# Optimization experiments

Measured on AMD Instinct MI355X. Metric: run time of the kernel, lower is better.

Reference implementation:

```python
import jax, jax.numpy as jnp
import numpy as np

D_MODEL = 1024
N_HEADS = 16
HEAD_DIM = D_MODEL // N_HEADS
SCALE = float(np.sqrt(HEAD_DIM))
NEG_INF = -1e30


def setup_inputs() -> dict:
    key = jax.random.key(0)
    k1, k2, k3 = jax.random.split(key, 3)
    B, S = 4, 2048
    x = jax.random.normal(k1, (B, S, D_MODEL), dtype=jnp.float32)
    attention_mask = jnp.ones((B, S), dtype=jnp.int32)
    # torch Linear(d, 3d, bias=False): y = x @ W^T; store pre-transposed (d, 3d)
    w_qkv = jax.random.normal(k2, (D_MODEL, 3 * D_MODEL), dtype=jnp.float32) * (1.0 / np.sqrt(D_MODEL))
    w_out = jax.random.normal(k3, (D_MODEL, D_MODEL), dtype=jnp.float32) * (1.0 / np.sqrt(D_MODEL))
    return {"x": x, "attention_mask": attention_mask, "w_qkv": w_qkv, "w_out": w_out}


def reference(x, attention_mask, w_qkv, w_out):
    B, S, _ = x.shape
    qkv = jnp.einsum('bsd,de->bse', x, w_qkv)                     # (B,S,3D)
    qkv = qkv.reshape(B, S, 3, N_HEADS, HEAD_DIM)
    q = qkv[:, :, 0].transpose(0, 2, 1, 3)                        # (B,H,S,hd)
    k = qkv[:, :, 1].transpose(0, 2, 1, 3)
    v = qkv[:, :, 2].transpose(0, 2, 1, 3)

    scores = jnp.einsum('bhqd,bhkd->bhqk', q, k) / SCALE          # (B,H,S,S)
    causal_mask = jnp.triu(jnp.ones((S, S), dtype=bool), k=1)     # True above diag
    scores = jnp.where(causal_mask[None, None], NEG_INF, scores)
    pad_mask = (attention_mask == 0)[:, None, None, :]            # (B,1,1,S)
    scores = jnp.where(pad_mask, NEG_INF, scores)

    attn = jax.nn.softmax(scores, axis=-1)                        # dropout=0 (eval)
    out = jnp.einsum('bhqk,bhkd->bhqd', attn, v)                  # (B,H,S,hd)
    out = out.transpose(0, 2, 1, 3).reshape(B, S, D_MODEL)
    return jnp.einsum('bsd,de->bse', out, w_out)
```

## Files before the change

kernel.cpp:

```cpp
#include <hip/hip_runtime.h>


typedef __attribute__((ext_vector_type(8))) short bf16x8;
typedef __attribute__((ext_vector_type(8))) unsigned short u16x8;
typedef __attribute__((ext_vector_type(4))) unsigned short u16x4;
typedef __attribute__((ext_vector_type(4))) float f32x4;

#define MFMA16 __builtin_amdgcn_mfma_f32_16x16x32_bf16

#define GLDS(gp, lp) __builtin_amdgcn_global_load_lds( \
    (const __attribute__((address_space(1))) unsigned int*)(gp), \
    (__attribute__((address_space(3))) unsigned int*)(lp), 16, 0, 0)

__device__ __forceinline__ unsigned short f2bf(float f) {
    union { float f; unsigned int u; } v; v.f = f;
    unsigned int r = v.u + 0x7fffu + ((v.u >> 16) & 1u);
    return (unsigned short)(r >> 16);
}

__global__ void k_prep(const float* __restrict__ x, unsigned short* __restrict__ xb,
                       const int* __restrict__ mask, unsigned short* __restrict__ mb,
                       const float* __restrict__ wqkv, unsigned short* __restrict__ w1t,
                       const float* __restrict__ wout, unsigned short* __restrict__ w2t) {
    __shared__ float tile[32][33];
    const int bx = blockIdx.x;
    if (bx < 4096) {
        size_t i = ((size_t)bx * 256 + threadIdx.x) * 8;
        float4 f0 = *(const float4*)(x + i);
        float4 f1 = *(const float4*)(x + i + 4);
        u16x8 v;
        v[0] = f2bf(f0.x); v[1] = f2bf(f0.y); v[2] = f2bf(f0.z); v[3] = f2bf(f0.w);
        v[4] = f2bf(f1.x); v[5] = f2bf(f1.y); v[6] = f2bf(f1.z); v[7] = f2bf(f1.w);
        *(u16x8*)(xb + i) = v;
        if (bx < 32) {
            int j = bx * 256 + threadIdx.x;
            mb[j] = mask[j] ? (unsigned short)0x3F80 : (unsigned short)0;
        }
    } else {
        const int b2 = bx - 4096;
        const int cb = b2 & 127, rb = b2 >> 7;
        const float* in = (cb < 96) ? wqkv : wout;
        unsigned short* out = (cb < 96) ? w1t : w2t;
        const int C = (cb < 96) ? 3072 : 1024;
        const int c0 = ((cb < 96) ? cb : cb - 96) * 32;
        const int r0 = rb * 32;
        int tx = threadIdx.x & 31, ty = threadIdx.x >> 5;
        for (int i = ty; i < 32; i += 8)
            tile[i][tx] = in[(size_t)(r0 + i) * C + (c0 + tx)];
        __syncthreads();
        for (int i = ty; i < 32; i += 8)
            out[(size_t)(c0 + i) * 1024 + (r0 + tx)] = f2bf(tile[tx][i]);
    }
}

template <int MODE>
__global__ __launch_bounds__(256) void k_gemm_bt(
    const unsigned short* __restrict__ Ab,
    const unsigned short* __restrict__ Bt,
    float* __restrict__ Cf,
    unsigned short* __restrict__ qb,
    unsigned short* __restrict__ kb,
    unsigned short* __restrict__ vt,
    const int* __restrict__ mask,
    int N, int K)
{
    __shared__ __align__(16) unsigned short la[128 * 64];
    __shared__ __align__(16) unsigned short lb[128 * 64];
    const int t = threadIdx.x;
    const int m0 = blockIdx.y * 128, n0 = blockIdx.x * 128;
    const int w = t >> 6, lane = t & 63;
    const int wm = (w & 1) * 64, wn = (w >> 1) * 64;
    const int lr = lane & 15, lq = lane >> 4;
    const int lr7 = lr & 7;
    const int rowb = lane >> 3;
    const int g8 = (((lane & 7) - rowb) & 7) * 8;

    f32x4 acc[4][4];
    for (int i = 0; i < 4; ++i)
        for (int j = 0; j < 4; ++j)
            acc[i][j] = (f32x4){0.f, 0.f, 0.f, 0.f};

    for (int k0 = 0; k0 < K; k0 += 64) {
        #pragma unroll
        for (int r = 0; r < 4; ++r) {
            const int rg = w * 8 + r * 32;
            GLDS(&Ab[(size_t)(m0 + rg + rowb) * K + k0 + g8], &la[rg * 64]);
            GLDS(&Bt[(size_t)(n0 + rg + rowb) * K + k0 + g8], &lb[rg * 64]);
        }
        __syncthreads();
        #pragma unroll
        for (int ks = 0; ks < 2; ++ks) {
            const int pa = ((ks * 4 + lq + lr7) & 7) * 8;
            bf16x8 af[4], bg[4];
            #pragma unroll
            for (int i = 0; i < 4; ++i) {
                af[i] = *(const bf16x8*)&la[(wm + i * 16 + lr) * 64 + pa];
                bg[i] = *(const bf16x8*)&lb[(wn + i * 16 + lr) * 64 + pa];
            }
            #pragma unroll
            for (int i = 0; i < 4; ++i)
                #pragma unroll
                for (int j = 0; j < 4; ++j)
                    acc[i][j] = MFMA16(af[i], bg[j], acc[i][j], 0, 0, 0);
        }
        __syncthreads();
    }

    const float QSCALE = 0.18033688f;
    if (MODE == 0) {
        for (int i = 0; i < 4; ++i)
            for (int j = 0; j < 4; ++j)
                for (int r = 0; r < 4; ++r) {
                    int row = m0 + wm + i * 16 + lq * 4 + r;
                    int col = n0 + wn + j * 16 + lr;
                    Cf[(size_t)row * N + col] = acc[i][j][r];
                }
    } else {
        const int which = n0 >> 10;
        if (which < 2) {
            unsigned short* dst = which ? kb : qb;
            const float sc = which ? 1.0f : QSCALE;
            for (int i = 0; i < 4; ++i)
                for (int j = 0; j < 4; ++j)
                    for (int r = 0; r < 4; ++r) {
                        int row = m0 + wm + i * 16 + lq * 4 + r;
                        int col = n0 + wn + j * 16 + lr;
                        int h = (col >> 6) & 15, d = col & 63;
                        int b = row >> 11, s = row & 2047;
                        dst[((size_t)(b * 16 + h) * 2048 + s) * 64 + d] = f2bf(acc[i][j][r] * sc);
                    }
        } else {
            for (int i = 0; i < 4; ++i) {
                int s0 = m0 + wm + i * 16 + lq * 4;
                int b = s0 >> 11, s = s0 & 2047;
                int4 m4 = *(const int4*)&mask[b * 2048 + s];
                for (int j = 0; j < 4; ++j) {
                    int col = n0 + wn + j * 16 + lr;
                    int h = (col >> 6) & 15, d = col & 63;
                    u16x4 pv;
                    pv[0] = m4.x ? f2bf(acc[i][j][0]) : (unsigned short)0;
                    pv[1] = m4.y ? f2bf(acc[i][j][1]) : (unsigned short)0;
                    pv[2] = m4.z ? f2bf(acc[i][j][2]) : (unsigned short)0;
                    pv[3] = m4.w ? f2bf(acc[i][j][3]) : (unsigned short)0;
                    *(u16x4*)&vt[((size_t)(b * 16 + h) * 64 + d) * 2048 + s] = pv;
                }
            }
        }
    }
}

__global__ __launch_bounds__(512, 4) void k_attn(
    const unsigned short* __restrict__ qb,
    const unsigned short* __restrict__ kb,
    const unsigned short* __restrict__ vt,
    const unsigned short* __restrict__ maskbg,
    unsigned short* __restrict__ ao)
{
    __shared__ __align__(16) unsigned short kt_lds[2][64 * 64];
    __shared__ __align__(16) unsigned short vt_lds[2][64 * 64];
    __shared__ __align__(16) unsigned short plds[8][16 * 72];

    const int t = threadIdx.x;
    const int w = t >> 6, lane = t & 63;
    const int lr = lane & 15, lq = lane >> 4;
    const int lr7 = lr & 7;
    const int bh = blockIdx.x, b = bh >> 4, h = bh & 15;

    const unsigned short* qp = qb + (size_t)bh * 2048 * 64;
    const unsigned short* kp = kb + (size_t)bh * 2048 * 64;
    const unsigned short* vp = vt + (size_t)bh * 64 * 2048;
    const unsigned short* mbg = maskbg + b * 2048;
    unsigned short* pw = plds[w];

    const int rowb = lane >> 3, c8 = lane & 7;
    const int sc8 = (c8 ^ rowb) * 8;

    auto stage = [&](int c) {
        const int buf = c & 1;
        const int k0 = c * 64;
        const int rg = 8 * w;
        const int row = rg + rowb;
        GLDS(&kp[(size_t)(k0 + row) * 64 + sc8], &kt_lds[buf][rg * 64]);
        GLDS(&vp[(size_t)row * 2048 + k0 + sc8], &vt_lds[buf][rg * 64]);
    };

    for (int pass = 0; pass < 2; ++pass) {
        const int stripe = pass ? (15 - (int)blockIdx.y) : (int)blockIdx.y;
        const int q0w = stripe * 128 + w * 16;

        bf16x8 aq0 = *(const bf16x8*)&qp[(q0w + lr) * 64 + lq * 8];
        bf16x8 aq1 = *(const bf16x8*)&qp[(q0w + lr) * 64 + 32 + lq * 8];

        f32x4 acc[4], lacc;
        lacc = (f32x4){0.f, 0.f, 0.f, 0.f};
        #pragma unroll
        for (int j = 0; j < 4; ++j) acc[j] = (f32x4){0.f, 0.f, 0.f, 0.f};

        const int nch = 2 * (stripe + 1);
        stage(0);
        for (int c = 0; c < nch; ++c) {
            __syncthreads();
            if (c + 1 < nch) stage(c + 1);
            const int k0 = c * 64;
            if (k0 < q0w + 16) {
                const unsigned short* kt = kt_lds[c & 1];
                const unsigned short* vtl = vt_lds[c & 1];
                const bool causal = (k0 + 63 > q0w);
                const int kcol0 = (lq ^ lr7) * 8;
                const int kcol1 = ((4 + lq) ^ lr7) * 8;
                #pragma unroll
                for (int ki = 0; ki < 4; ++ki) {
                    bf16x8 kf0 = *(const bf16x8*)&kt[(ki * 16 + lr) * 64 + kcol0];
                    bf16x8 kf1 = *(const bf16x8*)&kt[(ki * 16 + lr) * 64 + kcol1];
                    f32x4 s = (f32x4){0.f, 0.f, 0.f, 0.f};
                    s = MFMA16(kf0, aq0, s, 0, 0, 0);
                    s = MFMA16(kf1, aq1, s, 0, 0, 0);
                    unsigned int u[4];
                    #pragma unroll
                    for (int r = 0; r < 4; ++r) {
                        float scv = s[r];
                        if (causal) {
                            int key = k0 + ki * 16 + lq * 4 + r;
                            int qq  = q0w + lr;
                            scv = (key <= qq) ? scv : -3.0e38f;
                        }
                        float p = __builtin_amdgcn_exp2f(scv);
                        union { float f; unsigned int u; } cv; cv.f = p;
                        u[r] = cv.u;
                    }
                    uint2 pk;
                    pk.x = __builtin_amdgcn_perm(u[1], u[0], 0x07060302u);
                    pk.y = __builtin_amdgcn_perm(u[3], u[2], 0x07060302u);
                    *(uint2*)&pw[lr * 72 + ki * 16 + lq * 4] = pk;
                }
                #pragma unroll
                for (int kc = 0; kc < 64; kc += 32) {
                    bf16x8 pf = *(const bf16x8*)&pw[lr * 72 + kc + lq * 8];
                    bf16x8 mb = *(const bf16x8*)&mbg[k0 + kc + lq * 8];
                    const int vcol = (((kc >> 3) + lq) ^ lr7) * 8;
                    #pragma unroll
                    for (int j = 0; j < 4; ++j) {
                        bf16x8 vf = *(const bf16x8*)&vtl[(j * 16 + lr) * 64 + vcol];
                        acc[j] = MFMA16(pf, vf, acc[j], 0, 0, 0);
                    }
                    lacc = MFMA16(pf, mb, lacc, 0, 0, 0);
                }
            }
        }

        #pragma unroll
        for (int r = 0; r < 4; ++r) {
            float inv = 1.0f / fmaxf(lacc[r], 1e-30f);
            int row = q0w + lq * 4 + r;
            #pragma unroll
            for (int j = 0; j < 4; ++j) {
                int d = j * 16 + lr;
                ao[(size_t)(b * 2048 + row) * 1024 + h * 64 + d] = f2bf(acc[j][r] * inv);
            }
        }
        __syncthreads();
    }
}

extern "C" void kernel_launch(void* const* d_in, const int* in_sizes, int n_in,
                              void* d_out, int out_size, void* d_ws, size_t ws_size,
                              hipStream_t stream)
{
    const float* x    = (const float*)d_in[0];
    const int*   mask = (const int*)d_in[1];
    const float* wqkv = (const float*)d_in[2];
    const float* wout = (const float*)d_in[3];
    float* out = (float*)d_out;

    const size_t NEED = ((size_t)8192 * 1024 + (size_t)3072 * 1024 + (size_t)1024 * 1024 +
                         3 * (size_t)64 * 2048 * 64 + (size_t)8192 * 1024 + 8192) * 2;
    if (ws_size < NEED) return;

    char* ws = (char*)d_ws;
    unsigned short* xb  = (unsigned short*)ws; ws += (size_t)8192 * 1024 * 2;
    unsigned short* w1t = (unsigned short*)ws; ws += (size_t)3072 * 1024 * 2;
    unsigned short* w2t = (unsigned short*)ws; ws += (size_t)1024 * 1024 * 2;
    unsigned short* qb  = (unsigned short*)ws; ws += (size_t)64 * 2048 * 64 * 2;
    unsigned short* kb  = (unsigned short*)ws; ws += (size_t)64 * 2048 * 64 * 2;
    unsigned short* vt  = (unsigned short*)ws; ws += (size_t)64 * 64 * 2048 * 2;
    unsigned short* ao  = (unsigned short*)ws; ws += (size_t)8192 * 1024 * 2;
    unsigned short* mbg = (unsigned short*)ws; ws += (size_t)8192 * 2;

    k_prep<<<dim3(8192), 256, 0, stream>>>(x, xb, mask, mbg, wqkv, w1t, wout, w2t);
    k_gemm_bt<1><<<dim3(24, 64), 256, 0, stream>>>(xb, w1t, nullptr, qb, kb, vt, mask, 3072, 1024);
    k_attn<<<dim3(64, 8), 512, 0, stream>>>(qb, kb, vt, mbg, ao);
    k_gemm_bt<0><<<dim3(8, 64), 256, 0, stream>>>(ao, w2t, out, nullptr, nullptr, nullptr, nullptr, 1024, 1024);
}
```

Measured before the change: 246.9 us.

## Use 128x256 tiles with triple-buffered LDS pipeline and XCD-aware block remap in GEMMs

Both projection GEMMs move from 128x128 tiles with 256 threads to 128x256 tiles with 512 threads, staged through three LDS buffers. Global-to-LDS loads for tile k+2 are issued in halves inside the compute loop and gated by s_waitcnt vmcnt, so loads overlap MFMA work instead of stalling on the two __syncthreads per step. Block IDs are remapped (orig&7 striding) so neighbouring tiles land on the same XCD for L2 reuse, and setprio raises MFMA priority. In exchange, LDS per block is much larger (about 144KB), which limits occupancy, and the out-projection grid becomes small (256 blocks).

Measured after the change: 242.2 us. Within noise of the previous version (-1.9%).

```diff
diff --git a/kernel.cpp b/kernel.cpp
--- a/kernel.cpp
+++ b/kernel.cpp
@@ -53,8 +53,8 @@
     }
 }
 
-template <int MODE>
-__global__ __launch_bounds__(256) void k_gemm_bt(
+template <int MODE, int NBX>
+__global__ __launch_bounds__(512, 2) void k_gemm256(
     const unsigned short* __restrict__ Ab,
     const unsigned short* __restrict__ Bt,
     float* __restrict__ Cf,
@@ -64,46 +64,87 @@
     const int* __restrict__ mask,
     int N, int K)
 {
-    __shared__ __align__(16) unsigned short la[128 * 64];
-    __shared__ __align__(16) unsigned short lb[128 * 64];
+    __shared__ __align__(16) unsigned short la[3][128 * 64];
+    __shared__ __align__(16) unsigned short lb[3][256 * 64];
     const int t = threadIdx.x;
-    const int m0 = blockIdx.y * 128, n0 = blockIdx.x * 128;
     const int w = t >> 6, lane = t & 63;
-    const int wm = (w & 1) * 64, wn = (w >> 1) * 64;
     const int lr = lane & 15, lq = lane >> 4;
     const int lr7 = lr & 7;
-    const int rowb = lane >> 3;
-    const int g8 = (((lane & 7) - rowb) & 7) * 8;
+    const int rowb = lane >> 3, c8 = lane & 7;
+    const int g8 = ((c8 - rowb) & 7) * 8;
+
+    const int nwg = NBX * 64;
+    const int orig = blockIdx.y * NBX + blockIdx.x;
+    const int rm = (orig & 7) * (nwg >> 3) + (orig >> 3);
+    const int m0 = (rm / NBX) * 128;
+    const int n0 = (rm % NBX) * 256;
+
+    const int wm = (w >> 2) * 64;
+    const int wn = (w & 3) * 64;
+
+    const unsigned short* Arow = Ab + (size_t)(m0 + w * 8 + rowb) * K + g8;
+    const unsigned short* Brow = Bt + (size_t)(n0 + w * 8 + rowb) * K + g8;
+
+    auto stage3 = [&](int tt, int g) {
+        const int buf = tt % 3;
+        const size_t ko = (size_t)tt * 64;
+        if (g == 0) {
+            GLDS(Arow + ko,                    &la[buf][(w * 8) * 64]);
+            GLDS(Brow + ko,                    &lb[buf][(w * 8) * 64]);
+            GLDS(Brow + (size_t)64 * K + ko,   &lb[buf][(64 + w * 8) * 64]);
+        } else {
+            GLDS(Arow + (size_t)64 * K + ko,   &la[buf][(64 + w * 8) * 64]);
+            GLDS(Brow + (size_t)128 * K + ko,  &lb[buf][(128 + w * 8) * 64]);
+            GLDS(Brow + (size_t)192 * K + ko,  &lb[buf][(192 + w * 8) * 64]);
+        }
+    };
 
     f32x4 acc[4][4];
+    #pragma unroll
     for (int i = 0; i < 4; ++i)
+        #pragma unroll
         for (int j = 0; j < 4; ++j)
             acc[i][j] = (f32x4){0.f, 0.f, 0.f, 0.f};
 
-    for (int k0 = 0; k0 < K; k0 += 64) {
-        #pragma unroll
-        for (int r = 0; r < 4; ++r) {
-            const int rg = w * 8 + r * 32;
-            GLDS(&Ab[(size_t)(m0 + rg + rowb) * K + k0 + g8], &la[rg * 64]);
-            GLDS(&Bt[(size_t)(n0 + rg + rowb) * K + k0 + g8], &lb[rg * 64]);
-        }
-        __syncthreads();
+    const int nt = K >> 6;
+
+    stage3(0, 0); stage3(0, 1); stage3(1, 0); stage3(1, 1);
+    asm volatile("s_waitcnt vmcnt(6)" ::: "memory");
+    __builtin_amdgcn_sched_barrier(0);
+    __builtin_amdgcn_s_barrier();
+
+    for (int tt = 0; tt < nt; ++tt) {
+        const unsigned short* lat = la[tt % 3];
+        const unsigned short* lbt = lb[tt % 3];
         #pragma unroll
         for (int ks = 0; ks < 2; ++ks) {
             const int pa = ((ks * 4 + lq + lr7) & 7) * 8;
             bf16x8 af[4], bg[4];
             #pragma unroll
             for (int i = 0; i < 4; ++i) {
-                af[i] = *(const bf16x8*)&la[(wm + i * 16 + lr) * 64 + pa];
-                bg[i] = *(const bf16x8*)&lb[(wn + i * 16 + lr) * 64 + pa];
-            }
+                af[i] = *(const bf16x8*)&lat[(wm + i * 16 + lr) * 64 + pa];
+                bg[i] = *(const bf16x8*)&lbt[(wn + i * 16 + lr) * 64 + pa];
+            }
+            if (tt + 2 < nt) stage3(tt + 2, ks);
+            __builtin_amdgcn_s_barrier();
+            __builtin_amdgcn_s_setprio(1);
             #pragma unroll
             for (int i = 0; i < 4; ++i)
                 #pragma unroll
                 for (int j = 0; j < 4; ++j)
                     acc[i][j] = MFMA16(af[i], bg[j], acc[i][j], 0, 0, 0);
-        }
-        __syncthreads();
+            __builtin_amdgcn_s_setprio(0);
+            if (ks == 1) {
+                if (tt == nt - 2) {
+                    asm volatile("s_waitcnt vmcnt(0)" ::: "memory");
+                    __builtin_amdgcn_sched_barrier(0);
+                } else if (tt < nt - 2) {
+                    asm volatile("s_waitcnt vmcnt(6)" ::: "memory");
+                    __builtin_amdgcn_sched_barrier(0);
+                }
+            }
+            __builtin_amdgcn_s_barrier();
+        }
     }
 
     const float QSCALE = 0.18033688f;
@@ -287,7 +328,7 @@
     unsigned short* mbg = (unsigned short*)ws; ws += (size_t)8192 * 2;
 
     k_prep<<<dim3(8192), 256, 0, stream>>>(x, xb, mask, mbg, wqkv, w1t, wout, w2t);
-    k_gemm_bt<1><<<dim3(24, 64), 256, 0, stream>>>(xb, w1t, nullptr, qb, kb, vt, mask, 3072, 1024);
+    k_gemm256<1, 12><<<dim3(12, 64), 512, 0, stream>>>(xb, w1t, nullptr, qb, kb, vt, mask, 3072, 1024);
     k_attn<<<dim3(64, 8), 512, 0, stream>>>(qb, kb, vt, mbg, ao);
-    k_gemm_bt<0><<<dim3(8, 64), 256, 0, stream>>>(ao, w2t, out, nullptr, nullptr, nullptr, nullptr, 1024, 1024);
-}
+    k_gemm256<0, 4><<<dim3(4, 64), 512, 0, stream>>>(ao, w2t, out, nullptr, nullptr, nullptr, nullptr, 1024, 1024);
+}
```

## Process two query row-groups per wave in attention to reuse K/V fragments

Applied to the files above, without the earlier changes.

The attention kernel now runs 4 waves of 256 threads instead of 8 waves of 512, and each wave handles 32 query rows as two 16-row groups. K and V fragments loaded from LDS are shared across both groups, which halves LDS fragment reads per MFMA. Each thread now stages two rows of K and V per chunk. The cost is more registers per wave for the doubled accumulators and fewer waves per block, which lowers the parallelism available to hide latency. The causal skip granularity also becomes coarser.

After: 254.4 us. 1.03x slower.

```diff
diff --git a/kernel.cpp b/kernel.cpp
--- a/kernel.cpp
+++ b/kernel.cpp
@@ -149,7 +149,7 @@
     }
 }
 
-__global__ __launch_bounds__(512, 4) void k_attn(
+__global__ __launch_bounds__(256, 2) void k_attn(
     const unsigned short* __restrict__ qb,
     const unsigned short* __restrict__ kb,
     const unsigned short* __restrict__ vt,
@@ -158,7 +158,7 @@
 {
     __shared__ __align__(16) unsigned short kt_lds[2][64 * 64];
     __shared__ __align__(16) unsigned short vt_lds[2][64 * 64];
-    __shared__ __align__(16) unsigned short plds[8][16 * 72];
+    __shared__ __align__(16) unsigned short plds[4][32 * 72];
 
     const int t = threadIdx.x;
     const int w = t >> 6, lane = t & 63;
@@ -178,23 +178,30 @@
     auto stage = [&](int c) {
         const int buf = c & 1;
         const int k0 = c * 64;
-        const int rg = 8 * w;
+        const int rg = 16 * w;
         const int row = rg + rowb;
-        GLDS(&kp[(size_t)(k0 + row) * 64 + sc8], &kt_lds[buf][rg * 64]);
-        GLDS(&vp[(size_t)row * 2048 + k0 + sc8], &vt_lds[buf][rg * 64]);
+        GLDS(&kp[(size_t)(k0 + row) * 64 + sc8],       &kt_lds[buf][rg * 64]);
+        GLDS(&kp[(size_t)(k0 + row + 8) * 64 + sc8],   &kt_lds[buf][(rg + 8) * 64]);
+        GLDS(&vp[(size_t)row * 2048 + k0 + sc8],       &vt_lds[buf][rg * 64]);
+        GLDS(&vp[(size_t)(row + 8) * 2048 + k0 + sc8], &vt_lds[buf][(rg + 8) * 64]);
     };
 
     for (int pass = 0; pass < 2; ++pass) {
         const int stripe = pass ? (15 - (int)blockIdx.y) : (int)blockIdx.y;
-        const int q0w = stripe * 128 + w * 16;
-
-        bf16x8 aq0 = *(const bf16x8*)&qp[(q0w + lr) * 64 + lq * 8];
-        bf16x8 aq1 = *(const bf16x8*)&qp[(q0w + lr) * 64 + 32 + lq * 8];
-
-        f32x4 acc[4], lacc;
-        lacc = (f32x4){0.f, 0.f, 0.f, 0.f};
+        const int q0w = stripe * 128 + w * 32;
+
+        bf16x8 aq00 = *(const bf16x8*)&qp[(q0w + lr) * 64 + lq * 8];
+        bf16x8 aq01 = *(const bf16x8*)&qp[(q0w + lr) * 64 + 32 + lq * 8];
+        bf16x8 aq10 = *(const bf16x8*)&qp[(q0w + 16 + lr) * 64 + lq * 8];
+        bf16x8 aq11 = *(const bf16x8*)&qp[(q0w + 16 + lr) * 64 + 32 + lq * 8];
+
+        f32x4 acc[2][4], lacc[2];
         #pragma unroll
-        for (int j = 0; j < 4; ++j) acc[j] = (f32x4){0.f, 0.f, 0.f, 0.f};
+        for (int g = 0; g < 2; ++g) {
+            lacc[g] = (f32x4){0.f, 0.f, 0.f, 0.f};
+            #pragma unroll
+            for (int j = 0; j < 4; ++j) acc[g][j] = (f32x4){0.f, 0.f, 0.f, 0.f};
+        }
 
         const int nch = 2 * (stripe + 1);
         stage(0);
@@ -202,7 +209,7 @@
             __syncthreads();
             if (c + 1 < nch) stage(c + 1);
             const int k0 = c * 64;
-            if (k0 < q0w + 16) {
+            if (k0 < q0w + 32) {
                 const unsigned short* kt = kt_lds[c & 1];
                 const unsigned short* vtl = vt_lds[c & 1];
                 const bool causal = (k0 + 63 > q0w);
@@ -212,52 +219,62 @@
                 for (int ki = 0; ki < 4; ++ki) {
                     bf16x8 kf0 = *(const bf16x8*)&kt[(ki * 16 + lr) * 64 + kcol0];
                     bf16x8 kf1 = *(const bf16x8*)&kt[(ki * 16 + lr) * 64 + kcol1];
-                    f32x4 s = (f32x4){0.f, 0.f, 0.f, 0.f};
-                    s = MFMA16(kf0, aq0, s, 0, 0, 0);
-                    s = MFMA16(kf1, aq1, s, 0, 0, 0);
-                    unsigned int u[4];
                     #pragma unroll
-                    for (int r = 0; r < 4; ++r) {
-                        float scv = s[r];
-                        if (causal) {
-                            int key = k0 + ki * 16 + lq * 4 + r;
-                            int qq  = q0w + lr;
-                            scv = (key <= qq) ? scv : -3.0e38f;
+                    for (int g = 0; g < 2; ++g) {
+                        f32x4 s = (f32x4){0.f, 0.f, 0.f, 0.f};
+                        s = MFMA16(kf0, g ? aq10 : aq00, s, 0, 0, 0);
+                        s = MFMA16(kf1, g ? aq11 : aq01, s, 0, 0, 0);
+                        unsigned int u[4];
+                        #pragma unroll
+                        for (int r = 0; r < 4; ++r) {
+                            float scv = s[r];
+                            if (causal) {
+                                int key = k0 + ki * 16 + lq * 4 + r;
+                                int qq  = q0w + g * 16 + lr;
+                                scv = (key <= qq) ? scv : -3.0e38f;
+                            }
+                            float p = __builtin_amdgcn_exp2f(scv);
+                            union { float f; unsigned int u; } cv; cv.f = p;
+                            u[r] = cv.u;
                         }
-                        float p = __builtin_amdgcn_exp2f(scv);
-                        union { float f; unsigned int u; } cv; cv.f = p;
-                        u[r] = cv.u;
+                        uint2 pk;
+                        pk.x = __builtin_amdgcn_perm(u[1], u[0], 0x07060302u);
+                        pk.y = __builtin_amdgcn_perm(u[3], u[2], 0x07060302u);
+                        *(uint2*)&pw[(g * 16 + lr) * 72 + ki * 16 + lq * 4] = pk;
                     }
-                    uint2 pk;
-                    pk.x = __builtin_amdgcn_perm(u[1], u[0], 0x07060302u);
-                    pk.y = __builtin_amdgcn_perm(u[3], u[2], 0x07060302u);
-                    *(uint2*)&pw[lr * 72 + ki * 16 + lq * 4] = pk;
                 }
                 #pragma unroll
                 for (int kc = 0; kc < 64; kc += 32) {
-                    bf16x8 pf = *(const bf16x8*)&pw[lr * 72 + kc + lq * 8];
                     bf16x8 mb = *(const bf16x8*)&mbg[k0 + kc + lq * 8];
                     const int vcol = (((kc >> 3) + lq) ^ lr7) * 8;
+                    bf16x8 vf[4];
                     #pragma unroll
-                    for (int j = 0; j < 4; ++j) {
-                        bf16x8 vf = *(const bf16x8*)&vtl[(j * 16 + lr) * 64 + vcol];
-                        acc[j] = MFMA16(pf, vf, acc[j], 0, 0, 0);
+                    for (int j = 0; j < 4; ++j)
+                        vf[j] = *(const bf16x8*)&vtl[(j * 16 + lr) * 64 + vcol];
+                    #pragma unroll
+                    for (int g = 0; g < 2; ++g) {
+                        bf16x8 pf = *(const bf16x8*)&pw[(g * 16 + lr) * 72 + kc + lq * 8];
+                        #pragma unroll
+                        for (int j = 0; j < 4; ++j)
+                            acc[g][j] = MFMA16(pf, vf[j], acc[g][j], 0, 0, 0);
+                        lacc[g] = MFMA16(pf, mb, lacc[g], 0, 0, 0);
                     }
-                    lacc = MFMA16(pf, mb, lacc, 0, 0, 0);
                 }
             }
         }
 
         #pragma unroll
-        for (int r = 0; r < 4; ++r) {
-            float inv = 1.0f / fmaxf(lacc[r], 1e-30f);
-            int row = q0w + lq * 4 + r;
+        for (int g = 0; g < 2; ++g)
             #pragma unroll
-            for (int j = 0; j < 4; ++j) {
-                int d = j * 16 + lr;
-                ao[(size_t)(b * 2048 + row) * 1024 + h * 64 + d] = f2bf(acc[j][r] * inv);
+            for (int r = 0; r < 4; ++r) {
+                float inv = 1.0f / fmaxf(lacc[g][r], 1e-30f);
+                int row = q0w + g * 16 + lq * 4 + r;
+                #pragma unroll
+                for (int j = 0; j < 4; ++j) {
+                    int d = j * 16 + lr;
+                    ao[(size_t)(b * 2048 + row) * 1024 + h * 64 + d] = f2bf(acc[g][j][r] * inv);
+                }
             }
-        }
         __syncthreads();
     }
 }
@@ -288,6 +305,6 @@
 
     k_prep<<<dim3(8192), 256, 0, stream>>>(x, xb, mask, mbg, wqkv, w1t, wout, w2t);
     k_gemm_bt<1><<<dim3(24, 64), 256, 0, stream>>>(xb, w1t, nullptr, qb, kb, vt, mask, 3072, 1024);
-    k_attn<<<dim3(64, 8), 512, 0, stream>>>(qb, kb, vt, mbg, ao);
+    k_attn<<<dim3(64, 8), 256, 0, stream>>>(qb, kb, vt, mbg, ao);
     k_gemm_bt<0><<<dim3(8, 64), 256, 0, stream>>>(ao, w2t, out, nullptr, nullptr, nullptr, nullptr, 1024, 1024);
 }
```
